# Optimization experiments

Hardware: AMD Instinct MI355X
Metric: run time of the kernel (lower is better)

The kernel has to match this reference:

```python
import jax, jax.numpy as jnp
import numpy as np

B, T, C = 4, 1024, 2048
NH, HS = 16, 128          # n_head, head_size
NLQ, NLKV = 1536, 512     # q/kv latent dims
DHR = 64                  # rope head dim


def _rope(x, cos, sin):
    # x: [B, T, H, d]; cos/sin: [T, d//2]
    xr = x.reshape(x.shape[:-1] + (-1, 2))
    x_re, x_im = xr[..., 0], xr[..., 1]
    c = cos[None, :, None, :]
    s = sin[None, :, None, :]
    out = jnp.stack([x_re * c - x_im * s, x_re * s + x_im * c], axis=-1)
    return out.reshape(x.shape)


def setup_inputs() -> dict:
    key = jax.random.key(0)
    ks = jax.random.split(key, 10)
    w = 0.02  # init scale
    x = jax.random.normal(ks[0], (B, T, C), dtype=jnp.float32)
    # RoPE frequencies (standard theta=10000)
    inv_freq = 1.0 / (10000.0 ** (np.arange(0, DHR, 2, dtype=np.float32) / DHR))
    t = np.arange(T, dtype=np.float32)
    ang = np.outer(t, inv_freq)  # [T, DHR//2]
    cos = jnp.asarray(np.cos(ang), dtype=jnp.float32)
    sin = jnp.asarray(np.sin(ang), dtype=jnp.float32)
    return {
        "x": x,
        "cos": cos,
        "sin": sin,
        "W_dq": jax.random.normal(ks[1], (NLQ, C), jnp.float32) * w,
        "W_uq": jax.random.normal(ks[2], (C, NLQ), jnp.float32) * w,
        "W_dkv": jax.random.normal(ks[3], (NLKV, C), jnp.float32) * w,
        "W_uk": jax.random.normal(ks[4], (C, NLKV), jnp.float32) * w,
        "W_uv": jax.random.normal(ks[5], (C, NLKV), jnp.float32) * w,
        "W_qr": jax.random.normal(ks[6], (NH * DHR, NLQ), jnp.float32) * w,
        "W_kr": jax.random.normal(ks[7], (DHR, C), jnp.float32) * w,
        "W_o": jax.random.normal(ks[8], (C, C), jnp.float32) * w,
    }


def reference(x, cos, sin, W_dq, W_uq, W_dkv, W_uk, W_uv, W_qr, W_kr, W_o):
    # down-projected query latent: [B, T, NLQ]
    c_q = jnp.einsum('btc,qc->btq', x, W_dq)
    # absorbed matrices (training-path math, identical to inference buffers)
    # W_uq.weight [C, NLQ] viewed flat as (NLQ, NH, HS) then heads first
    k_eff = jnp.einsum('hqd,hdk->hqk',
                       W_uq.reshape(NLQ, NH, HS).transpose(1, 0, 2),
                       W_uk.reshape(NH, HS, NLKV))           # [NH, NLQ, NLKV]
    v_eff = (W_uv.T @ W_o.T).reshape(NLKV, NH, HS).transpose(1, 0, 2)  # [NH, NLKV, HS]
    # kv latent: [B, T, NLKV]
    c_kv = jnp.einsum('btc,kc->btk', x, W_dkv)
    # content scores via absorbed matmuls: [B, NH, T, T]
    q_abs = jnp.einsum('btq,hqk->bhtk', c_q, k_eff)
    attn_c = jnp.einsum('bhtk,bsk->bhts', q_abs, c_kv)
    # decoupled RoPE branch
    c_kr = jnp.einsum('btc,dc->btd', x, W_kr)[:, :, None, :]   # [B,T,1,DHR]
    k_r = _rope(c_kr, cos, sin)[:, :, 0, :]                     # [B,T,DHR]
    c_qr = jnp.einsum('btq,rq->btr', c_q, W_qr).reshape(B, T, NH, DHR)
    q_r = _rope(c_qr, cos, sin)                                 # [B,T,NH,DHR]
    attn_r = jnp.einsum('bthd,bsd->bhts', q_r, k_r)             # [B,NH,T,T]
    attn = (attn_c + attn_r) / jnp.sqrt(jnp.float32(HS + DHR))
    # causal mask
    mask = jnp.tril(jnp.ones((T, T), dtype=bool))
    attn = jnp.where(mask[None, None], attn, jnp.float32(-jnp.inf))
    attn = jax.nn.softmax(attn, axis=-1)
    # output via absorbed value/output projection
    y_lat = jnp.einsum('bhts,bsk->bhtk', attn, c_kv)            # [B,NH,T,NLKV]
    y = jnp.einsum('bhtk,hkd->bthd', y_lat, v_eff).reshape(B, T, C)
    return y
```

## Files before the change

### kernel.cpp

```cpp
#include <hip/hip_runtime.h>
#include <type_traits>

typedef unsigned short ushort_t;
typedef unsigned int   uint_t;
typedef __attribute__((ext_vector_type(8))) short bf16x8;
typedef __attribute__((ext_vector_type(4))) float f32x4;

constexpr int Bn = 4, Tn = 1024, Cn = 2048, NH = 16, HS = 128;
constexpr int NLQ = 1536, NLKV = 512, DHR = 64;
constexpr int BT = Bn * Tn;
constexpr int KLD = 640;
constexpr float ATT_SCALE = 0.07216878364870323f;
constexpr float LOG2E = 1.4426950408889634f;

__device__ __forceinline__ ushort_t f2bf(float f) {
    uint_t u = __float_as_uint(f);
    u += 0x7fffu + ((u >> 16) & 1u);
    return (ushort_t)(u >> 16);
}

__device__ __forceinline__ void gload_lds16(const void* g, void* l) {
    __builtin_amdgcn_global_load_lds(
        (__attribute__((address_space(1))) void*)g,
        (__attribute__((address_space(3))) void*)l, 16, 0, 0);
}

template<typename OutT>
__device__ __forceinline__ void gemm_tile128(
    const ushort_t* __restrict__ Ab, int lda,
    const ushort_t* __restrict__ Bb, int ldb,
    OutT* __restrict__ Cb, int ldc, int K,
    ushort_t* As, ushort_t* Bs)
{
    constexpr int BK = 32;
    const int tid  = threadIdx.x;
    const int lane = tid & 63;
    const int w    = tid >> 6;
    const int l15 = lane & 15, l4 = lane >> 4;
    const int wr = w >> 1, wc = w & 1;
    const int srow = lane >> 2;
    const int scol = (lane & 3) * 8;

    f32x4 acc[4][4];
    #pragma unroll
    for (int m = 0; m < 4; ++m)
        #pragma unroll
        for (int n = 0; n < 4; ++n) acc[m][n] = (f32x4){0.f, 0.f, 0.f, 0.f};

    for (int k0 = 0; k0 < K; k0 += BK) {
        #pragma unroll
        for (int i = 0; i < 2; ++i) {
            int r = w * 32 + i * 16;
            gload_lds16(Ab + (long)(r + srow) * lda + k0 + scol, &As[r * BK]);
            gload_lds16(Bb + (long)(r + srow) * ldb + k0 + scol, &Bs[r * BK]);
        }
        __syncthreads();

        bf16x8 af[4], bfv[4];
        #pragma unroll
        for (int m = 0; m < 4; ++m)
            af[m] = *(const bf16x8*)&As[(wr * 64 + m * 16 + l15) * BK + l4 * 8];
        #pragma unroll
        for (int n = 0; n < 4; ++n)
            bfv[n] = *(const bf16x8*)&Bs[(wc * 64 + n * 16 + l15) * BK + l4 * 8];
        #pragma unroll
        for (int m = 0; m < 4; ++m)
            #pragma unroll
            for (int n = 0; n < 4; ++n)
                acc[m][n] = __builtin_amdgcn_mfma_f32_16x16x32_bf16(af[m], bfv[n], acc[m][n], 0, 0, 0);
        __syncthreads();
    }

    #pragma unroll
    for (int m = 0; m < 4; ++m)
        #pragma unroll
        for (int j = 0; j < 4; ++j) {
            long row = wr * 64 + m * 16 + l4 * 4 + j;
            #pragma unroll
            for (int n = 0; n < 4; ++n) {
                long col = wc * 64 + n * 16 + l15;
                if constexpr (std::is_same<OutT, float>::value)
                    Cb[row * ldc + col] = acc[m][n][j];
                else
                    Cb[row * ldc + col] = f2bf(acc[m][n][j]);
            }
        }
}

template<typename OutT>
__global__ __launch_bounds__(256, 2) void gemm_bf16(
    const ushort_t* __restrict__ A, const ushort_t* __restrict__ B,
    OutT* __restrict__ C,
    int K, int lda, int ldb, int ldc)
{
    __shared__ ushort_t As[128 * 32];
    __shared__ ushort_t Bs[128 * 32];
    const ushort_t* Ab = A + (long)blockIdx.y * 128 * lda;
    const ushort_t* Bb = B + (long)blockIdx.x * 128 * ldb;
    OutT*           Cb = C + (long)blockIdx.y * 128 * ldc + (long)blockIdx.x * 128;
    gemm_tile128<OutT>(Ab, lda, Bb, ldb, Cb, ldc, K, As, Bs);
}

__global__ __launch_bounds__(256, 2) void gemm_split(
    const ushort_t* __restrict__ A, int lda, int K,
    const ushort_t* __restrict__ B,
    ushort_t* __restrict__ C1, int ldc1, int split,
    ushort_t* __restrict__ C2, int ldc2)
{
    __shared__ ushort_t As[128 * 32];
    __shared__ ushort_t Bs[128 * 32];
    const int nt = blockIdx.x, mt = blockIdx.y;
    const ushort_t* Ab = A + (long)mt * 128 * lda;
    const ushort_t* Bb = B + (long)nt * 128 * K;
    ushort_t* Cb; int ldc;
    if (nt < split) { Cb = C1 + (long)mt * 128 * ldc1 + nt * 128;           ldc = ldc1; }
    else            { Cb = C2 + (long)mt * 128 * ldc2 + (nt - split) * 128; ldc = ldc2; }
    gemm_tile128<ushort_t>(Ab, lda, Bb, K, Cb, ldc, K, As, Bs);
}

__global__ __launch_bounds__(256, 2) void attn_s_gemm(
    const ushort_t* __restrict__ qnom, const ushort_t* __restrict__ qrb,
    const ushort_t* __restrict__ kabs, const ushort_t* __restrict__ kfull,
    ushort_t* __restrict__ Spk)
{
    __shared__ ushort_t As[128 * 32];
    __shared__ ushort_t Bs[128 * 32];
    const int id  = blockIdx.x;
    const int sid = (id & 7) * 288 + (id >> 3);
    const int x = sid % 36, z = sid / 36;
    int ti = 0;
    while ((ti + 1) * (ti + 2) / 2 <= x) ++ti;
    const int si = x - ti * (ti + 1) / 2;
    const int h = z >> 2, b = z & 3;

    const int tid  = threadIdx.x;
    const int lane = tid & 63;
    const int w    = tid >> 6;
    const int l15 = lane & 15, l4 = lane >> 4;
    const int wr = w >> 1, wc = w & 1;
    const int srow = lane >> 2;
    const int scol = (lane & 3) * 8;

    const ushort_t* A1 = qnom + ((long)(b * 1024 + ti * 128)) * 2048 + h * 128;
    const ushort_t* A2 = qrb  + ((long)(b * 1024 + ti * 128)) * 1024 + h * 64;
    const ushort_t* B1 = kabs + ((long)(b * 1024 + si * 128)) * 2048 + h * 128;
    const ushort_t* B2 = kfull + ((long)(b * 1024 + si * 128)) * KLD + 512;
    ushort_t* Cb = Spk + (long)z * 589824 + (long)x * 16384;

    f32x4 acc[4][4];
    #pragma unroll
    for (int m = 0; m < 4; ++m)
        #pragma unroll
        for (int n = 0; n < 4; ++n) acc[m][n] = (f32x4){0.f, 0.f, 0.f, 0.f};

    #pragma unroll
    for (int kk = 0; kk < 6; ++kk) {
        const bool qa = (kk < 4);
        const ushort_t* Asrc = qa ? A1 + kk * 32 : A2 + kk * 32 - 128;
        const ushort_t* Bsrc = qa ? B1 + kk * 32 : B2 + kk * 32 - 128;
        const int ldA = qa ? 2048 : 1024;
        const int ldB = qa ? 2048 : KLD;
        #pragma unroll
        for (int i = 0; i < 2; ++i) {
            int r = w * 32 + i * 16;
            gload_lds16(Asrc + (long)(r + srow) * ldA + scol, &As[r * 32]);
            gload_lds16(Bsrc + (long)(r + srow) * ldB + scol, &Bs[r * 32]);
        }
        __syncthreads();

        bf16x8 af[4], bfv[4];
        #pragma unroll
        for (int m = 0; m < 4; ++m)
            af[m] = *(const bf16x8*)&As[(wr * 64 + m * 16 + l15) * 32 + l4 * 8];
        #pragma unroll
        for (int n = 0; n < 4; ++n)
            bfv[n] = *(const bf16x8*)&Bs[(wc * 64 + n * 16 + l15) * 32 + l4 * 8];
        #pragma unroll
        for (int m = 0; m < 4; ++m)
            #pragma unroll
            for (int n = 0; n < 4; ++n)
                acc[m][n] = __builtin_amdgcn_mfma_f32_16x16x32_bf16(af[m], bfv[n], acc[m][n], 0, 0, 0);
        __syncthreads();
    }

    #pragma unroll
    for (int m = 0; m < 4; ++m)
        #pragma unroll
        for (int j = 0; j < 4; ++j) {
            long row = wr * 64 + m * 16 + l4 * 4 + j;
            #pragma unroll
            for (int n = 0; n < 4; ++n)
                Cb[row * 128 + wc * 64 + n * 16 + l15] = f2bf(acc[m][n][j]);
        }
}

__global__ __launch_bounds__(256) void attn_softmax(ushort_t* __restrict__ Spk)
{
    const int wid  = threadIdx.x >> 6;
    const int lane = threadIdx.x & 63;
    const int r = blockIdx.x * 4 + wid;
    const int z = r >> 10, t = r & 1023;
    const int ti = t >> 7;
    const int nc = ti + 1;
    ushort_t* base = Spk + (long)z * 589824 + (long)(ti * (ti + 1) / 2) * 16384
                        + (t & 127) * 128;
    const float SCL = ATT_SCALE * LOG2E;

    float p0[8], p1[8];
    float mx = -INFINITY;
    #pragma unroll
    for (int c = 0; c < 8; ++c) {
        p0[c] = -INFINITY; p1[c] = -INFINITY;
        if (c < nc) {
            uint_t u = *(const uint_t*)&base[c * 16384 + lane * 2];
            int kv = c * 128 + lane * 2;
            float a  = __uint_as_float(u << 16);
            float bb = __uint_as_float(u & 0xffff0000u);
            if (kv     <= t) p0[c] = a  * SCL;
            if (kv + 1 <= t) p1[c] = bb * SCL;
            mx = fmaxf(mx, fmaxf(p0[c], p1[c]));
        }
    }
    #pragma unroll
    for (int off = 32; off >= 1; off >>= 1) mx = fmaxf(mx, __shfl_xor(mx, off));
    float s = 0.f;
    #pragma unroll
    for (int c = 0; c < 8; ++c) {
        p0[c] = exp2f(p0[c] - mx);
        p1[c] = exp2f(p1[c] - mx);
        if (c < nc) s += p0[c] + p1[c];
    }
    #pragma unroll
    for (int off = 32; off >= 1; off >>= 1) s += __shfl_xor(s, off);
    const float inv = 1.f / s;
    #pragma unroll
    for (int c = 0; c < 8; ++c) if (c < nc) {
        uint_t o = (uint_t)f2bf(p0[c] * inv) | ((uint_t)f2bf(p1[c] * inv) << 16);
        *(uint_t*)&base[c * 16384 + lane * 2] = o;
    }
}

__global__ __launch_bounds__(256, 2) void attn_pv_gemm(
    const ushort_t* __restrict__ Spk, const ushort_t* __restrict__ VeffT,
    float* __restrict__ out)
{
    __shared__ ushort_t As[128 * 32];
    __shared__ ushort_t Bs[128 * 32];
    const int id  = blockIdx.x;
    const int sid = (id & 7) * 64 + (id >> 3);
    const int ti = sid & 7, z = sid >> 3;
    const int tid  = threadIdx.x;
    const int lane = tid & 63;
    const int w    = tid >> 6;
    const int l15 = lane & 15, l4 = lane >> 4;
    const int wr = w >> 1, wc = w & 1;
    const int srow = lane >> 2;
    const int scol = (lane & 3) * 8;
    const int h = z >> 2, b = z & 3;
    const int K = (ti + 1) * 128;
    const ushort_t* Abase = Spk + (long)z * 589824 + (long)(ti * (ti + 1) / 2) * 16384;
    const ushort_t* Bb = VeffT + ((long)b * 2048 + h * 128) * 1024;
    float* Cb = out + ((long)b * 1024 + ti * 128) * 2048 + h * 128;

    f32x4 acc[4][4];
    #pragma unroll
    for (int m = 0; m < 4; ++m)
        #pragma unroll
        for (int n = 0; n < 4; ++n) acc[m][n] = (f32x4){0.f, 0.f, 0.f, 0.f};

    for (int k0 = 0; k0 < K; k0 += 32) {
        const ushort_t* At = Abase + (k0 >> 7) * 16384 + (k0 & 127);
        #pragma unroll
        for (int i = 0; i < 2; ++i) {
            int r = w * 32 + i * 16;
            gload_lds16(At + (long)(r + srow) * 128 + scol, &As[r * 32]);
            gload_lds16(Bb + (long)(r + srow) * 1024 + k0 + scol, &Bs[r * 32]);
        }
        __syncthreads();

        bf16x8 af[4], bfv[4];
        #pragma unroll
        for (int m = 0; m < 4; ++m)
            af[m] = *(const bf16x8*)&As[(wr * 64 + m * 16 + l15) * 32 + l4 * 8];
        #pragma unroll
        for (int n = 0; n < 4; ++n)
            bfv[n] = *(const bf16x8*)&Bs[(wc * 64 + n * 16 + l15) * 32 + l4 * 8];
        #pragma unroll
        for (int m = 0; m < 4; ++m)
            #pragma unroll
            for (int n = 0; n < 4; ++n)
                acc[m][n] = __builtin_amdgcn_mfma_f32_16x16x32_bf16(af[m], bfv[n], acc[m][n], 0, 0, 0);
        __syncthreads();
    }

    #pragma unroll
    for (int m = 0; m < 4; ++m)
        #pragma unroll
        for (int j = 0; j < 4; ++j) {
            long row = wr * 64 + m * 16 + l4 * 4 + j;
            #pragma unroll
            for (int n = 0; n < 4; ++n)
                Cb[row * 2048 + wc * 64 + n * 16 + l15] = acc[m][n][j];
        }
}

__global__ void cvt_all(const float* __restrict__ x,   const float* __restrict__ Wdq,
                        const float* __restrict__ Wdkv, const float* __restrict__ Wkr,
                        const float* __restrict__ Wqr,  const float* __restrict__ Wo,
                        const float* __restrict__ Wuk,
                        ushort_t* __restrict__ xb, ushort_t* __restrict__ WB1,
                        ushort_t* __restrict__ WB2, ushort_t* __restrict__ Wo_b,
                        ushort_t* __restrict__ WB3)
{
    const int bid = blockIdx.x;
    const float* src = nullptr; ushort_t* dst;
    if      (bid < 4096) { src = x    + (long)bid * 2048;          dst = xb   + (long)bid * 2048; }
    else if (bid < 5632) { long b = bid - 4096; src = Wdq  + b * 2048; dst = WB1 + b * 2048; }
    else if (bid < 6144) { long b = bid - 5632; src = Wdkv + b * 2048; dst = WB1 + 3145728 + b * 2048; }
    else if (bid < 6208) { long b = bid - 6144; src = Wkr  + b * 2048; dst = WB1 + 4194304 + b * 2048; }
    else if (bid < 6272) { long b = bid - 6208;                        dst = WB1 + 4325376 + b * 2048; }
    else if (bid < 7040) { long b = bid - 6272; src = Wqr  + b * 2048; dst = WB2 + 3145728 + b * 2048; }
    else if (bid < 9088) { long b = bid - 7040; src = Wo   + b * 2048; dst = Wo_b + b * 2048; }
    else                 { long b = bid - 9088; src = Wuk  + b * 2048; dst = WB3 + b * 2048; }

    const long i = (long)threadIdx.x * 8;
    if (!src) { *(uint4*)&dst[i] = make_uint4(0, 0, 0, 0); return; }
    float4 a = *(const float4*)&src[i];
    float4 b4 = *(const float4*)&src[i + 4];
    ushort_t p[8] = {f2bf(a.x), f2bf(a.y), f2bf(a.z), f2bf(a.w),
                     f2bf(b4.x), f2bf(b4.y), f2bf(b4.z), f2bf(b4.w)};
    *(uint4*)&dst[i] = *(const uint4*)p;
}

__global__ __launch_bounds__(256) void transcvt_g(
    const float* __restrict__ in, ushort_t* __restrict__ out, int ldin, int R)
{
    __shared__ float tile[64][65];
    const int c0 = blockIdx.x * 64, r0 = blockIdx.y * 64;
    const int t = threadIdx.x;
    #pragma unroll
    for (int i = 0; i < 4; ++i) {
        int idx = t + i * 256;
        int r = idx >> 4, c4 = idx & 15;
        float4 v = *(const float4*)&in[(long)(r0 + r) * ldin + c0 + c4 * 4];
        tile[r][c4 * 4 + 0] = v.x; tile[r][c4 * 4 + 1] = v.y;
        tile[r][c4 * 4 + 2] = v.z; tile[r][c4 * 4 + 3] = v.w;
    }
    __syncthreads();
    #pragma unroll
    for (int i = 0; i < 4; ++i) {
        int idx = t + i * 256;
        int c = idx >> 4, r4 = idx & 15;
        ushort_t p[4];
        #pragma unroll
        for (int j = 0; j < 4; ++j) p[j] = f2bf(tile[r4 * 4 + j][c]);
        *(uint2*)&out[(long)(c0 + c) * R + r0 + r4 * 4] = *(const uint2*)p;
    }
}

__global__ void rope_kr_kernel(ushort_t* __restrict__ kfull,
                               const float* __restrict__ cosT, const float* __restrict__ sinT) {
    int p = blockIdx.x * 256 + threadIdx.x;
    if (p >= BT * 32) return;
    int bt = p >> 5, i = p & 31;
    int t = bt & (Tn - 1);
    float c = cosT[t * 32 + i], s = sinT[t * 32 + i];
    uint_t u = *(const uint_t*)&kfull[(long)bt * KLD + 512 + 2 * i];
    float re = __uint_as_float(u << 16);
    float im = __uint_as_float(u & 0xffff0000u);
    float o0 = re * c - im * s, o1 = re * s + im * c;
    uint_t o = (uint_t)f2bf(o0) | ((uint_t)f2bf(o1) << 16);
    *(uint_t*)&kfull[(long)bt * KLD + 512 + 2 * i] = o;
}

__global__ void rope_qr_kernel(ushort_t* __restrict__ qrb,
                               const float* __restrict__ cosT, const float* __restrict__ sinT) {
    int p = blockIdx.x * 256 + threadIdx.x;
    if (p >= BT * 512) return;
    int bt = p >> 9, rem = p & 511;
    int hh = rem >> 5, i = rem & 31;
    int t = bt & (Tn - 1);
    float c = cosT[t * 32 + i], s = sinT[t * 32 + i];
    long off = (long)bt * 1024 + hh * 64 + 2 * i;
    uint_t u = *(const uint_t*)&qrb[off];
    float re = __uint_as_float(u << 16);
    float im = __uint_as_float(u & 0xffff0000u);
    float o0 = re * c - im * s, o1 = re * s + im * c;
    uint_t o = (uint_t)f2bf(o0) | ((uint_t)f2bf(o1) << 16);
    *(uint_t*)&qrb[off] = o;
}

__global__ void transpose_veff(const ushort_t* __restrict__ Veff, ushort_t* __restrict__ VeffT) {
    int idx = blockIdx.x * 256 + threadIdx.x;
    int c = idx & 2047, rest = idx >> 11;
    int t8 = rest & 127, b = rest >> 7;
    ushort_t v[8];
    #pragma unroll
    for (int j = 0; j < 8; ++j)
        v[j] = Veff[((long)b * Tn + t8 * 8 + j) * 2048 + c];
    *(uint4*)&VeffT[((long)b * 2048 + c) * Tn + t8 * 8] = *(const uint4*)v;
}

extern "C" void kernel_launch(void* const* d_in, const int* in_sizes, int n_in,
                              void* d_out, int out_size, void* d_ws, size_t ws_size,
                              hipStream_t stream)
{
    (void)in_sizes; (void)n_in; (void)out_size; (void)ws_size;
    const float* x     = (const float*)d_in[0];
    const float* cosT  = (const float*)d_in[1];
    const float* sinT  = (const float*)d_in[2];
    const float* W_dq  = (const float*)d_in[3];
    const float* W_uq  = (const float*)d_in[4];
    const float* W_dkv = (const float*)d_in[5];
    const float* W_uk  = (const float*)d_in[6];
    const float* W_uv  = (const float*)d_in[7];
    const float* W_qr  = (const float*)d_in[8];
    const float* W_kr  = (const float*)d_in[9];
    const float* W_o   = (const float*)d_in[10];
    float* out = (float*)d_out;

    ushort_t* ws = (ushort_t*)d_ws;
    ushort_t* xb     = ws;
    ushort_t* WB1    = ws + 8388608;
    ushort_t* WB2    = ws + 12845056;
    ushort_t* Wo_b   = ws + 17563648;
    ushort_t* WuvT_b = ws + 21757952;
    ushort_t* cq_b   = ws + 22806528;
    ushort_t* WB3    = ws + 29097984;
    ushort_t* Veff   = ws + 31195136;
    ushort_t* Spk    = ws;
    ushort_t* qnom   = ws + 39583744;
    ushort_t* qr_b   = ws + 47972352;
    ushort_t* kabs   = ws + 52166656;
    ushort_t* kfull  = ws + 60555264;
    ushort_t* VeffT  = ws + 63176704;
    ushort_t* Mtb    = WB3 + 1048576;

    dim3 blk(256, 1, 1);

    cvt_all<<<dim3(9600), blk, 0, stream>>>(x, W_dq, W_dkv, W_kr, W_qr, W_o, W_uk,
                                            xb, WB1, WB2, Wo_b, WB3);
    transcvt_g<<<dim3(32, 24), blk, 0, stream>>>(W_uq, WB2, 2048, 1536);
    transcvt_g<<<dim3(8, 32), blk, 0, stream>>>(W_uv, WuvT_b, 512, 2048);

    gemm_bf16<ushort_t><<<dim3(4, 16, 1), blk, 0, stream>>>(
        Wo_b, WuvT_b, Mtb, Cn, Cn, Cn, NLKV);

    gemm_split<<<dim3(17, 32, 1), blk, 0, stream>>>(
        xb, Cn, Cn, WB1, cq_b, NLQ, 12, kfull, KLD);
    rope_kr_kernel<<<dim3(BT*32/256), blk, 0, stream>>>(kfull, cosT, sinT);

    gemm_split<<<dim3(24, 32, 1), blk, 0, stream>>>(
        cq_b, NLQ, NLQ, WB2, qnom, Cn, 16, qr_b, NH*DHR);
    rope_qr_kernel<<<dim3(BT*512/256), blk, 0, stream>>>(qr_b, cosT, sinT);

    gemm_split<<<dim3(32, 32, 1), blk, 0, stream>>>(
        kfull, KLD, NLKV, WB3, kabs, Cn, 16, Veff, Cn);
    transpose_veff<<<dim3(4096), blk, 0, stream>>>(Veff, VeffT);

    attn_s_gemm<<<dim3(2304, 1, 1), blk, 0, stream>>>(qnom, qr_b, kabs, kfull, Spk);
    attn_softmax<<<dim3(BT * NH / 4), blk, 0, stream>>>(Spk);
    attn_pv_gemm<<<dim3(512, 1, 1), blk, 0, stream>>>(Spk, VeffT, out);
}
```

Baseline: 310.8 us.

## Triple-buffer LDS tiles with one barrier per step in all GEMMs

Every GEMM kernel now keeps three LDS buffers per operand. Each step issues the global-to-LDS loads two K-steps ahead, then uses a partial vmcnt wait and a single barrier in place of two __syncthreads, so memory latency overlaps with MFMA work. The gemm_split kernels also move to a 1D grid with an XCD-interleaved block remapping to improve L2 locality. The cost is three times the LDS per block (48KB), which may limit occupancy. The vmcnt(4) count assumes exactly four outstanding loads per stage.

Measured after the change: 314.2 us. Within noise of the previous version (+1.1%).

```diff
diff --git a/kernel.cpp b/kernel.cpp
--- a/kernel.cpp
+++ b/kernel.cpp
@@ -25,14 +25,20 @@
         (__attribute__((address_space(3))) void*)l, 16, 0, 0);
 }
 
+__device__ __forceinline__ void pipe_wait(bool last) {
+    if (last) asm volatile("s_waitcnt vmcnt(0)" ::: "memory");
+    else      asm volatile("s_waitcnt vmcnt(4)" ::: "memory");
+    __builtin_amdgcn_s_barrier();
+    asm volatile("" ::: "memory");
+}
+
 template<typename OutT>
-__device__ __forceinline__ void gemm_tile128(
+__device__ __forceinline__ void gemm_tile128_pipe(
     const ushort_t* __restrict__ Ab, int lda,
     const ushort_t* __restrict__ Bb, int ldb,
     OutT* __restrict__ Cb, int ldc, int K,
     ushort_t* As, ushort_t* Bs)
 {
-    constexpr int BK = 32;
     const int tid  = threadIdx.x;
     const int lane = tid & 63;
     const int w    = tid >> 6;
@@ -40,35 +46,45 @@
     const int wr = w >> 1, wc = w & 1;
     const int srow = lane >> 2;
     const int scol = (lane & 3) * 8;
-
-    f32x4 acc[4][4];
-    #pragma unroll
-    for (int m = 0; m < 4; ++m)
-        #pragma unroll
-        for (int n = 0; n < 4; ++n) acc[m][n] = (f32x4){0.f, 0.f, 0.f, 0.f};
-
-    for (int k0 = 0; k0 < K; k0 += BK) {
+    const int nT = K >> 5;
+
+    auto stage = [&](int t) {
+        const int buf = t % 3;
+        const int k0 = t * 32;
         #pragma unroll
         for (int i = 0; i < 2; ++i) {
             int r = w * 32 + i * 16;
-            gload_lds16(Ab + (long)(r + srow) * lda + k0 + scol, &As[r * BK]);
-            gload_lds16(Bb + (long)(r + srow) * ldb + k0 + scol, &Bs[r * BK]);
-        }
-        __syncthreads();
+            gload_lds16(Ab + (long)(r + srow) * lda + k0 + scol, &As[buf * 4096 + r * 32]);
+            gload_lds16(Bb + (long)(r + srow) * ldb + k0 + scol, &Bs[buf * 4096 + r * 32]);
+        }
+    };
+
+    f32x4 acc[4][4];
+    #pragma unroll
+    for (int m = 0; m < 4; ++m)
+        #pragma unroll
+        for (int n = 0; n < 4; ++n) acc[m][n] = (f32x4){0.f, 0.f, 0.f, 0.f};
+
+    stage(0);
+    if (nT > 1) stage(1);
+
+    for (int t = 0; t < nT; ++t) {
+        pipe_wait(t + 1 >= nT);
+        if (t + 2 < nT) stage(t + 2);
+        const int buf = t % 3;
 
         bf16x8 af[4], bfv[4];
         #pragma unroll
         for (int m = 0; m < 4; ++m)
-            af[m] = *(const bf16x8*)&As[(wr * 64 + m * 16 + l15) * BK + l4 * 8];
+            af[m] = *(const bf16x8*)&As[buf * 4096 + (wr * 64 + m * 16 + l15) * 32 + l4 * 8];
         #pragma unroll
         for (int n = 0; n < 4; ++n)
-            bfv[n] = *(const bf16x8*)&Bs[(wc * 64 + n * 16 + l15) * BK + l4 * 8];
+            bfv[n] = *(const bf16x8*)&Bs[buf * 4096 + (wc * 64 + n * 16 + l15) * 32 + l4 * 8];
         #pragma unroll
         for (int m = 0; m < 4; ++m)
             #pragma unroll
             for (int n = 0; n < 4; ++n)
                 acc[m][n] = __builtin_amdgcn_mfma_f32_16x16x32_bf16(af[m], bfv[n], acc[m][n], 0, 0, 0);
-        __syncthreads();
     }
 
     #pragma unroll
@@ -93,29 +109,31 @@
     OutT* __restrict__ C,
     int K, int lda, int ldb, int ldc)
 {
-    __shared__ ushort_t As[128 * 32];
-    __shared__ ushort_t Bs[128 * 32];
+    __shared__ ushort_t As[3 * 4096];
+    __shared__ ushort_t Bs[3 * 4096];
     const ushort_t* Ab = A + (long)blockIdx.y * 128 * lda;
     const ushort_t* Bb = B + (long)blockIdx.x * 128 * ldb;
     OutT*           Cb = C + (long)blockIdx.y * 128 * ldc + (long)blockIdx.x * 128;
-    gemm_tile128<OutT>(Ab, lda, Bb, ldb, Cb, ldc, K, As, Bs);
+    gemm_tile128_pipe<OutT>(Ab, lda, Bb, ldb, Cb, ldc, K, As, Bs);
 }
 
 __global__ __launch_bounds__(256, 2) void gemm_split(
-    const ushort_t* __restrict__ A, int lda, int K,
+    const ushort_t* __restrict__ A, int lda, int K, int ntiles,
     const ushort_t* __restrict__ B,
     ushort_t* __restrict__ C1, int ldc1, int split,
     ushort_t* __restrict__ C2, int ldc2)
 {
-    __shared__ ushort_t As[128 * 32];
-    __shared__ ushort_t Bs[128 * 32];
-    const int nt = blockIdx.x, mt = blockIdx.y;
+    __shared__ ushort_t As[3 * 4096];
+    __shared__ ushort_t Bs[3 * 4096];
+    const int id  = blockIdx.x;
+    const int sid = (id & 7) * (gridDim.x >> 3) + (id >> 3);
+    const int nt = sid % ntiles, mt = sid / ntiles;
     const ushort_t* Ab = A + (long)mt * 128 * lda;
     const ushort_t* Bb = B + (long)nt * 128 * K;
     ushort_t* Cb; int ldc;
     if (nt < split) { Cb = C1 + (long)mt * 128 * ldc1 + nt * 128;           ldc = ldc1; }
     else            { Cb = C2 + (long)mt * 128 * ldc2 + (nt - split) * 128; ldc = ldc2; }
-    gemm_tile128<ushort_t>(Ab, lda, Bb, K, Cb, ldc, K, As, Bs);
+    gemm_tile128_pipe<ushort_t>(Ab, lda, Bb, K, Cb, ldc, K, As, Bs);
 }
 
 __global__ __launch_bounds__(256, 2) void attn_s_gemm(
@@ -123,8 +141,8 @@
     const ushort_t* __restrict__ kabs, const ushort_t* __restrict__ kfull,
     ushort_t* __restrict__ Spk)
 {
-    __shared__ ushort_t As[128 * 32];
-    __shared__ ushort_t Bs[128 * 32];
+    __shared__ ushort_t As[3 * 4096];
+    __shared__ ushort_t Bs[3 * 4096];
     const int id  = blockIdx.x;
     const int sid = (id & 7) * 288 + (id >> 3);
     const int x = sid % 36, z = sid / 36;
@@ -147,40 +165,43 @@
     const ushort_t* B2 = kfull + ((long)(b * 1024 + si * 128)) * KLD + 512;
     ushort_t* Cb = Spk + (long)z * 589824 + (long)x * 16384;
 
-    f32x4 acc[4][4];
-    #pragma unroll
-    for (int m = 0; m < 4; ++m)
-        #pragma unroll
-        for (int n = 0; n < 4; ++n) acc[m][n] = (f32x4){0.f, 0.f, 0.f, 0.f};
-
-    #pragma unroll
-    for (int kk = 0; kk < 6; ++kk) {
-        const bool qa = (kk < 4);
-        const ushort_t* Asrc = qa ? A1 + kk * 32 : A2 + kk * 32 - 128;
-        const ushort_t* Bsrc = qa ? B1 + kk * 32 : B2 + kk * 32 - 128;
-        const int ldA = qa ? 2048 : 1024;
-        const int ldB = qa ? 2048 : KLD;
+    auto stage = [&](int t) {
+        const int buf = t % 3;
+        const ushort_t* Asrc; const ushort_t* Bsrc; int ldA, ldB;
+        if (t < 4) { Asrc = A1 + t * 32;       Bsrc = B1 + t * 32;       ldA = 2048; ldB = 2048; }
+        else       { Asrc = A2 + (t - 4) * 32; Bsrc = B2 + (t - 4) * 32; ldA = 1024; ldB = KLD; }
         #pragma unroll
         for (int i = 0; i < 2; ++i) {
             int r = w * 32 + i * 16;
-            gload_lds16(Asrc + (long)(r + srow) * ldA + scol, &As[r * 32]);
-            gload_lds16(Bsrc + (long)(r + srow) * ldB + scol, &Bs[r * 32]);
-        }
-        __syncthreads();
-
+            gload_lds16(Asrc + (long)(r + srow) * ldA + scol, &As[buf * 4096 + r * 32]);
+            gload_lds16(Bsrc + (long)(r + srow) * ldB + scol, &Bs[buf * 4096 + r * 32]);
+        }
+    };
+
+    f32x4 acc[4][4];
+    #pragma unroll
+    for (int m = 0; m < 4; ++m)
+        #pragma unroll
+        for (int n = 0; n < 4; ++n) acc[m][n] = (f32x4){0.f, 0.f, 0.f, 0.f};
+
+    stage(0); stage(1);
+    #pragma unroll
+    for (int t = 0; t < 6; ++t) {
+        pipe_wait(t == 5);
+        if (t + 2 < 6) stage(t + 2);
+        const int buf = t % 3;
         bf16x8 af[4], bfv[4];
         #pragma unroll
         for (int m = 0; m < 4; ++m)
-            af[m] = *(const bf16x8*)&As[(wr * 64 + m * 16 + l15) * 32 + l4 * 8];
+            af[m] = *(const bf16x8*)&As[buf * 4096 + (wr * 64 + m * 16 + l15) * 32 + l4 * 8];
         #pragma unroll
         for (int n = 0; n < 4; ++n)
-            bfv[n] = *(const bf16x8*)&Bs[(wc * 64 + n * 16 + l15) * 32 + l4 * 8];
+            bfv[n] = *(const bf16x8*)&Bs[buf * 4096 + (wc * 64 + n * 16 + l15) * 32 + l4 * 8];
         #pragma unroll
         for (int m = 0; m < 4; ++m)
             #pragma unroll
             for (int n = 0; n < 4; ++n)
                 acc[m][n] = __builtin_amdgcn_mfma_f32_16x16x32_bf16(af[m], bfv[n], acc[m][n], 0, 0, 0);
-        __syncthreads();
     }
 
     #pragma unroll
@@ -244,8 +265,8 @@
     const ushort_t* __restrict__ Spk, const ushort_t* __restrict__ VeffT,
     float* __restrict__ out)
 {
-    __shared__ ushort_t As[128 * 32];
-    __shared__ ushort_t Bs[128 * 32];
+    __shared__ ushort_t As[3 * 4096];
+    __shared__ ushort_t Bs[3 * 4096];
     const int id  = blockIdx.x;
     const int sid = (id & 7) * 64 + (id >> 3);
     const int ti = sid & 7, z = sid >> 3;
@@ -257,40 +278,46 @@
     const int srow = lane >> 2;
     const int scol = (lane & 3) * 8;
     const int h = z >> 2, b = z & 3;
-    const int K = (ti + 1) * 128;
+    const int nT = (ti + 1) * 4;
     const ushort_t* Abase = Spk + (long)z * 589824 + (long)(ti * (ti + 1) / 2) * 16384;
     const ushort_t* Bb = VeffT + ((long)b * 2048 + h * 128) * 1024;
     float* Cb = out + ((long)b * 1024 + ti * 128) * 2048 + h * 128;
 
-    f32x4 acc[4][4];
-    #pragma unroll
-    for (int m = 0; m < 4; ++m)
-        #pragma unroll
-        for (int n = 0; n < 4; ++n) acc[m][n] = (f32x4){0.f, 0.f, 0.f, 0.f};
-
-    for (int k0 = 0; k0 < K; k0 += 32) {
+    auto stage = [&](int t) {
+        const int buf = t % 3;
+        const int k0 = t * 32;
         const ushort_t* At = Abase + (k0 >> 7) * 16384 + (k0 & 127);
         #pragma unroll
         for (int i = 0; i < 2; ++i) {
             int r = w * 32 + i * 16;
-            gload_lds16(At + (long)(r + srow) * 128 + scol, &As[r * 32]);
-            gload_lds16(Bb + (long)(r + srow) * 1024 + k0 + scol, &Bs[r * 32]);
-        }
-        __syncthreads();
-
+            gload_lds16(At + (long)(r + srow) * 128 + scol, &As[buf * 4096 + r * 32]);
+            gload_lds16(Bb + (long)(r + srow) * 1024 + k0 + scol, &Bs[buf * 4096 + r * 32]);
+        }
+    };
+
+    f32x4 acc[4][4];
+    #pragma unroll
+    for (int m = 0; m < 4; ++m)
+        #pragma unroll
+        for (int n = 0; n < 4; ++n) acc[m][n] = (f32x4){0.f, 0.f, 0.f, 0.f};
+
+    stage(0); stage(1);
+    for (int t = 0; t < nT; ++t) {
+        pipe_wait(t + 1 >= nT);
+        if (t + 2 < nT) stage(t + 2);
+        const int buf = t % 3;
         bf16x8 af[4], bfv[4];
         #pragma unroll
         for (int m = 0; m < 4; ++m)
-            af[m] = *(const bf16x8*)&As[(wr * 64 + m * 16 + l15) * 32 + l4 * 8];
+            af[m] = *(const bf16x8*)&As[buf * 4096 + (wr * 64 + m * 16 + l15) * 32 + l4 * 8];
         #pragma unroll
         for (int n = 0; n < 4; ++n)
-            bfv[n] = *(const bf16x8*)&Bs[(wc * 64 + n * 16 + l15) * 32 + l4 * 8];
+            bfv[n] = *(const bf16x8*)&Bs[buf * 4096 + (wc * 64 + n * 16 + l15) * 32 + l4 * 8];
         #pragma unroll
         for (int m = 0; m < 4; ++m)
             #pragma unroll
             for (int n = 0; n < 4; ++n)
                 acc[m][n] = __builtin_amdgcn_mfma_f32_16x16x32_bf16(af[m], bfv[n], acc[m][n], 0, 0, 0);
-        __syncthreads();
     }
 
     #pragma unroll
@@ -446,19 +473,19 @@
     gemm_bf16<ushort_t><<<dim3(4, 16, 1), blk, 0, stream>>>(
         Wo_b, WuvT_b, Mtb, Cn, Cn, Cn, NLKV);
 
-    gemm_split<<<dim3(17, 32, 1), blk, 0, stream>>>(
-        xb, Cn, Cn, WB1, cq_b, NLQ, 12, kfull, KLD);
+    gemm_split<<<dim3(544), blk, 0, stream>>>(
+        xb, Cn, Cn, 17, WB1, cq_b, NLQ, 12, kfull, KLD);
     rope_kr_kernel<<<dim3(BT*32/256), blk, 0, stream>>>(kfull, cosT, sinT);
 
-    gemm_split<<<dim3(24, 32, 1), blk, 0, stream>>>(
-        cq_b, NLQ, NLQ, WB2, qnom, Cn, 16, qr_b, NH*DHR);
+    gemm_split<<<dim3(768), blk, 0, stream>>>(
+        cq_b, NLQ, NLQ, 24, WB2, qnom, Cn, 16, qr_b, NH*DHR);
     rope_qr_kernel<<<dim3(BT*512/256), blk, 0, stream>>>(qr_b, cosT, sinT);
 
-    gemm_split<<<dim3(32, 32, 1), blk, 0, stream>>>(
-        kfull, KLD, NLKV, WB3, kabs, Cn, 16, Veff, Cn);
+    gemm_split<<<dim3(1024), blk, 0, stream>>>(
+        kfull, KLD, NLKV, 32, WB3, kabs, Cn, 16, Veff, Cn);
     transpose_veff<<<dim3(4096), blk, 0, stream>>>(Veff, VeffT);
 
-    attn_s_gemm<<<dim3(2304, 1, 1), blk, 0, stream>>>(qnom, qr_b, kabs, kfull, Spk);
+    attn_s_gemm<<<dim3(2304), blk, 0, stream>>>(qnom, qr_b, kabs, kfull, Spk);
     attn_softmax<<<dim3(BT * NH / 4), blk, 0, stream>>>(Spk);
-    attn_pv_gemm<<<dim3(512, 1, 1), blk, 0, stream>>>(Spk, VeffT, out);
-}
+    attn_pv_gemm<<<dim3(512), blk, 0, stream>>>(Spk, VeffT, out);
+}
```
